# Kernel tuning notes

Measured on AMD Instinct MI355X. Metric: run time of the kernel, lower is better.

The kernel has to match this reference:

```python
import jax, jax.numpy as jnp
import numpy as np
import math

DIM = 1024
N_HEADS = 16
HEAD_DIM = DIM // N_HEADS


def rope(x):
    # x: [B, H, S, D] with D == HEAD_DIM, interleaved even/odd rotation
    S = x.shape[-2]
    D = x.shape[-1]
    pos = jnp.arange(S, dtype=x.dtype)[:, None]              # [S, 1]
    dim = jnp.arange(D // 2, dtype=x.dtype)[None, :]         # [1, D/2]
    theta = pos / jnp.exp(2.0 * dim / D * math.log(10000.0))  # [S, D/2]
    sin = jnp.sin(theta)[None, None]                          # [1,1,S,D/2]
    cos = jnp.cos(theta)[None, None]
    x1 = x[..., ::2]
    x2 = x[..., 1::2]
    out1 = x1 * cos - x2 * sin
    out2 = x1 * sin + x2 * cos
    # interleave back: stack on last axis then flatten pairs
    return jnp.stack([out1, out2], axis=-1).reshape(x.shape)


def setup_inputs() -> dict:
    key = jax.random.key(0)
    ks = jax.random.split(key, 9)
    B, S = 2, 2048
    s = 1.0 / math.sqrt(DIM)
    inp = {
        "x": jax.random.normal(ks[0], (B, S, DIM), dtype=jnp.float32),
        "wq": jax.random.normal(ks[1], (DIM, DIM), dtype=jnp.float32) * s,
        "bq": jnp.zeros((DIM,), dtype=jnp.float32),
        "wk": jax.random.normal(ks[2], (DIM, DIM), dtype=jnp.float32) * s,
        "bk": jnp.zeros((DIM,), dtype=jnp.float32),
        "wv": jax.random.normal(ks[3], (DIM, DIM), dtype=jnp.float32) * s,
        "bv": jnp.zeros((DIM,), dtype=jnp.float32),
        "wo": jax.random.normal(ks[4], (DIM, DIM), dtype=jnp.float32) * s,
        "bo": jnp.zeros((DIM,), dtype=jnp.float32),
    }
    return inp


def reference(x, wq, bq, wk, bk, wv, bv, wo, bo):
    B, S, _ = x.shape
    # torch Linear: y = x @ W^T + b
    def proj(w, b):
        y = jnp.einsum('bsd,ed->bse', x, w) + b
        return y.reshape(B, S, N_HEADS, HEAD_DIM).transpose(0, 2, 1, 3)  # [B,H,S,Dh]
    q = rope(proj(wq, bq))
    k = rope(proj(wk, bk))
    v = proj(wv, bv)
    score = jnp.einsum('bhqd,bhkd->bhqk', q, k) / math.sqrt(HEAD_DIM)
    causal = jnp.tril(jnp.ones((S, S), dtype=bool))
    score = jnp.where(causal[None, None], score, -jnp.inf)
    attn = jax.nn.softmax(score, axis=-1)
    out = jnp.einsum('bhqk,bhkd->bhqd', attn, v)
    out = out.transpose(0, 2, 1, 3).reshape(B, S, DIM)
    return jnp.einsum('bsd,ed->bse', out, wo) + bo
```

## Files before the change

kernel.cpp:

```cpp
#include <hip/hip_runtime.h>
#include <cstdint>
#include <cstddef>
#include <cmath>


typedef __bf16 bf16_t;
typedef __bf16 bf16x8 __attribute__((ext_vector_type(8)));
typedef __bf16 bf16x4 __attribute__((ext_vector_type(4)));
typedef float  f32x4  __attribute__((ext_vector_type(4)));

#define DEVFN __device__ __forceinline__

static constexpr int Bn  = 2;
static constexpr int S   = 2048;
static constexpr int DIM = 1024;
static constexpr int NH  = 16;
static constexpr int HD  = 64;
static constexpr int Mrows = Bn * S;

DEVFN f32x4 mfma16(bf16x8 a, bf16x8 b, f32x4 c) {
  return __builtin_amdgcn_mfma_f32_16x16x32_bf16(a, b, c, 0, 0, 0);
}

DEVFN void gl_lds16(const bf16_t* g, bf16_t* l) {
  __builtin_amdgcn_global_load_lds(
      (const __attribute__((address_space(1))) unsigned*)g,
      (__attribute__((address_space(3))) unsigned*)l, 16, 0, 0);
}

DEVFN float fast_exp2(float x) { return exp2f(x); }

__global__ __launch_bounds__(256) void k_prep(
    const float* __restrict__ x, const float* __restrict__ wq,
    const float* __restrict__ wk, const float* __restrict__ wv,
    const float* __restrict__ wo, bf16_t* __restrict__ xb,
    bf16_t* __restrict__ wqb, bf16_t* __restrict__ wkb,
    bf16_t* __restrict__ wvb, bf16_t* __restrict__ wob,
    float2* __restrict__ tab) {
  const int bid = blockIdx.x;
  if (bid < 8192) {
    const float* src;
    bf16_t* dst;
    size_t base;
    if (bid < 4096) {
      src = x; dst = xb; base = (size_t)bid << 10;
    } else {
      int wsel = (bid - 4096) >> 10;
      src = wsel == 0 ? wq : wsel == 1 ? wk : wsel == 2 ? wv : wo;
      dst = wsel == 0 ? wqb : wsel == 1 ? wkb : wsel == 2 ? wvb : wob;
      base = (size_t)((bid - 4096) & 1023) << 10;
    }
    size_t i = base + (size_t)threadIdx.x * 4;
    float4 v = *(const float4*)(src + i);
    bf16x4 o = { (bf16_t)v.x, (bf16_t)v.y, (bf16_t)v.z, (bf16_t)v.w };
    *(bf16x4*)(dst + i) = o;
  } else {
    int i = (bid - 8192) * 256 + threadIdx.x;
    int s = i >> 5, d = i & 31;
    float th = (float)s * expf((float)d * -0.2878231366f);
    tab[i] = make_float2(cosf(th), sinf(th));
  }
}

__global__ __launch_bounds__(256) void k_rope(bf16_t* __restrict__ X,
                                              const float2* __restrict__ tab,
                                              float scale) {
  int i = blockIdx.x * 256 + threadIdx.x;
  int row = i >> 7;
  int s = row & (S - 1);
  int dd = (i & 7) << 3;
  int p0 = dd >> 1;
  bf16x8 v = *(bf16x8*)(X + (size_t)i * 8);
  bf16x8 o;
#pragma unroll
  for (int j = 0; j < 4; ++j) {
    float x1 = (float)v[2 * j], x2 = (float)v[2 * j + 1];
    float2 cs = tab[s * 32 + p0 + j];
    o[2 * j]     = (bf16_t)((x1 * cs.x - x2 * cs.y) * scale);
    o[2 * j + 1] = (bf16_t)((x1 * cs.y + x2 * cs.x) * scale);
  }
  *(bf16x8*)(X + (size_t)i * 8) = o;
}

__global__ __launch_bounds__(256) void k_trans(const bf16_t* __restrict__ Vin,
                                               bf16_t* __restrict__ VT) {
  __shared__ __align__(16) bf16_t tile[64][72];
  int s0 = blockIdx.x * 64, bh = blockIdx.y;
  int b = bh >> 4, h = bh & 15;
  int t = threadIdx.x;
#pragma unroll
  for (int it = 0; it < 2; ++it) {
    int sl = (t >> 3) + it * 32, d0 = (t & 7) << 3;
    *(bf16x8*)&tile[sl][d0] =
        *(const bf16x8*)(Vin + (size_t)(b * S + s0 + sl) * DIM + h * HD + d0);
  }
  __syncthreads();
  int d = t >> 2, c0 = (t & 3) * 16;
  bf16_t buf[16];
#pragma unroll
  for (int j = 0; j < 16; ++j) buf[j] = tile[c0 + j][d];
  bf16_t* op = VT + ((size_t)bh * HD + d) * S + s0 + c0;
  *(bf16x8*)op = *(bf16x8*)&buf[0];
  *(bf16x8*)(op + 8) = *(bf16x8*)&buf[8];
}

DEVFN void stage64(const bf16_t* __restrict__ A, const bf16_t* __restrict__ Bw,
                   bf16_t* Al, bf16_t* Bl, int m0, int n0, int k0, int t,
                   int w) {
#pragma unroll
  for (int ld = 0; ld < 4; ++ld) {
    int c = t + ld * 256;
    int row = c >> 3;
    int j = ((c & 7) ^ (row & 7)) << 3;
    bf16_t* dstA = Al + (size_t)(w * 64 + ld * 256) * 8;
    bf16_t* dstB = Bl + (size_t)(w * 64 + ld * 256) * 8;
    gl_lds16(A + (size_t)(m0 + row) * DIM + k0 + j, dstA);
    gl_lds16(Bw + (size_t)(n0 + row) * DIM + k0 + j, dstB);
  }
}

__global__ __launch_bounds__(256) void k_gemm_qkv(
    const bf16_t* __restrict__ A, const bf16_t* __restrict__ Wall,
    const float* __restrict__ c0, const float* __restrict__ c1,
    const float* __restrict__ c2, bf16_t* __restrict__ Oq,
    bf16_t* __restrict__ Ok, bf16_t* __restrict__ Ov_) {
  __shared__ __align__(16) bf16_t Al[128 * 64];
  __shared__ __align__(16) bf16_t Bl[128 * 64];
  const int t = threadIdx.x, w = t >> 6, l = t & 63;
  const int lr = l & 15, lc = l >> 4;
  const int lid = blockIdx.x;
  const int xcd = lid & 7, s = lid >> 3;
  const int my = ((xcd >> 1) << 3) + (s & 7);
  const int nx = (xcd & 1) * 12 + (s >> 3);
  const int m0 = my * 128, n0g = nx * 128;
  const int z = n0g >> 10, n0l = n0g & 1023;
  const int wr = w >> 1, wc = w & 1;
  f32x4 acc[4][4] = {};

  for (int k0 = 0; k0 < DIM; k0 += 64) {
    __syncthreads();
    stage64(A, Wall, Al, Bl, m0, n0g, k0, t, w);
    asm volatile("s_waitcnt vmcnt(0)" ::: "memory");
    __syncthreads();
    bf16x8 af[2][4], bfr[2][4];
#pragma unroll
    for (int ks = 0; ks < 2; ++ks) {
#pragma unroll
      for (int mi = 0; mi < 4; ++mi) {
        int row = wr * 64 + mi * 16 + lr;
        int off = ((ks * 4 + lc) << 4) ^ ((row & 7) << 4);
        af[ks][mi] = *(const bf16x8*)((const char*)Al + row * 128 + off);
      }
#pragma unroll
      for (int ni = 0; ni < 4; ++ni) {
        int row = wc * 64 + ni * 16 + lr;
        int off = ((ks * 4 + lc) << 4) ^ ((row & 7) << 4);
        bfr[ks][ni] = *(const bf16x8*)((const char*)Bl + row * 128 + off);
      }
    }
    __builtin_amdgcn_s_setprio(1);
#pragma unroll
    for (int ks = 0; ks < 2; ++ks)
#pragma unroll
      for (int mi = 0; mi < 4; ++mi)
#pragma unroll
        for (int ni = 0; ni < 4; ++ni)
          acc[mi][ni] = mfma16(af[ks][mi], bfr[ks][ni], acc[mi][ni]);
    __builtin_amdgcn_s_setprio(0);
  }

  bf16_t* Ov = z == 0 ? Oq : (z == 1 ? Ok : Ov_);
  const float* bias = z == 0 ? c0 : (z == 1 ? c1 : c2);
#pragma unroll
  for (int ni = 0; ni < 4; ++ni) {
    const int col = n0l + wc * 64 + ni * 16 + lr;
    const float bv = bias[col];
#pragma unroll
    for (int mi = 0; mi < 4; ++mi)
#pragma unroll
      for (int r = 0; r < 4; ++r) {
        int row = m0 + wr * 64 + mi * 16 + lc * 4 + r;
        Ov[(size_t)row * DIM + col] = (bf16_t)(acc[mi][ni][r] + bv);
      }
  }
}

__global__ __launch_bounds__(256) void k_gemm_out(
    const bf16_t* __restrict__ A, const bf16_t* __restrict__ Bw,
    const float* __restrict__ bias, float* __restrict__ Ov) {
  __shared__ __align__(16) bf16_t Al[128 * 64];
  __shared__ __align__(16) bf16_t Bl[128 * 64];
  const int t = threadIdx.x, w = t >> 6, l = t & 63;
  const int lr = l & 15, lc = l >> 4;
  const int lid = blockIdx.x;
  const int xcd = lid & 7, s = lid >> 3;
  const int my = ((xcd >> 1) << 3) + (s & 7);
  const int nx = (xcd & 1) * 4 + (s >> 3);
  const int m0 = my * 128, n0 = nx * 128;
  const int wr = w >> 1, wc = w & 1;
  f32x4 acc[4][4] = {};

  for (int k0 = 0; k0 < DIM; k0 += 64) {
    __syncthreads();
    stage64(A, Bw, Al, Bl, m0, n0, k0, t, w);
    asm volatile("s_waitcnt vmcnt(0)" ::: "memory");
    __syncthreads();
    bf16x8 af[2][4], bfr[2][4];
#pragma unroll
    for (int ks = 0; ks < 2; ++ks) {
#pragma unroll
      for (int mi = 0; mi < 4; ++mi) {
        int row = wr * 64 + mi * 16 + lr;
        int off = ((ks * 4 + lc) << 4) ^ ((row & 7) << 4);
        af[ks][mi] = *(const bf16x8*)((const char*)Al + row * 128 + off);
      }
#pragma unroll
      for (int ni = 0; ni < 4; ++ni) {
        int row = wc * 64 + ni * 16 + lr;
        int off = ((ks * 4 + lc) << 4) ^ ((row & 7) << 4);
        bfr[ks][ni] = *(const bf16x8*)((const char*)Bl + row * 128 + off);
      }
    }
    __builtin_amdgcn_s_setprio(1);
#pragma unroll
    for (int ks = 0; ks < 2; ++ks)
#pragma unroll
      for (int mi = 0; mi < 4; ++mi)
#pragma unroll
        for (int ni = 0; ni < 4; ++ni)
          acc[mi][ni] = mfma16(af[ks][mi], bfr[ks][ni], acc[mi][ni]);
    __builtin_amdgcn_s_setprio(0);
  }

#pragma unroll
  for (int ni = 0; ni < 4; ++ni) {
    int col = n0 + wc * 64 + ni * 16 + lr;
    float bv = bias[col];
#pragma unroll
    for (int mi = 0; mi < 4; ++mi)
#pragma unroll
      for (int r = 0; r < 4; ++r) {
        int row = m0 + wr * 64 + mi * 16 + lc * 4 + r;
        Ov[(size_t)row * DIM + col] = acc[mi][ni][r] + bv;
      }
  }
}

DEVFN void stage_kv(const bf16_t* __restrict__ Kc,
                    const bf16_t* __restrict__ VT, bf16_t* Kb, bf16_t* Vb,
                    int b, int bh, int h, int k0, int tid, int w) {
#pragma unroll
  for (int ld = 0; ld < 2; ++ld) {
    int c = tid + ld * 256;
    int row = c >> 3;
    int j = ((c & 7) ^ (row & 7)) << 3;
    bf16_t* dstK = Kb + (size_t)(w * 64 + ld * 256) * 8;
    bf16_t* dstV = Vb + (size_t)(w * 64 + ld * 256) * 8;
    gl_lds16(Kc + (size_t)(b * S + k0 + row) * DIM + h * HD + j, dstK);
    gl_lds16(VT + ((size_t)bh * HD + row) * S + k0 + j, dstV);
  }
}

__global__ __launch_bounds__(256) void k_attn(const bf16_t* __restrict__ Q,
                                              const bf16_t* __restrict__ Kc,
                                              const bf16_t* __restrict__ VT,
                                              bf16_t* __restrict__ O) {
  __shared__ __align__(16) bf16_t Kl[2][64 * 64];
  __shared__ __align__(16) bf16_t Vl[2][64 * 64];
  __shared__ __align__(16) bf16_t Pl[4][16 * 64];
  const int tid = threadIdx.x, w = tid >> 6, l = tid & 63;
  const int lr = l & 15, lc = l >> 4;
  const int lid = blockIdx.x;
  const int xcd = lid & 7;
  const int rest = lid >> 3;
  const int t_ord = rest >> 2;
  const int hh = rest & 3;
  const int tile = 31 - t_ord;
  const int bh = xcd * 4 + hh;
  const int b = bh >> 4, h = bh & 15;
  char* Pw = (char*)&Pl[w][0];

  const int q0 = tile * 64;
  const int nt = tile + 1;

  bf16x8 qf[2];
  {
    const bf16_t* qp =
        Q + (size_t)(b * S + q0 + w * 16 + lr) * DIM + h * HD + lc * 8;
    qf[0] = *(const bf16x8*)qp;
    qf[1] = *(const bf16x8*)(qp + 32);
  }
  f32x4 o[4] = {};
  float m_run = -INFINITY;
  float rowsum = 0.f;

  stage_kv(Kc, VT, &Kl[0][0], &Vl[0][0], b, bh, h, 0, tid, w);

#pragma unroll 1
  for (int it = 0; it < nt; ++it) {
    const int cur = it & 1;
    const bf16_t* Kb = &Kl[cur][0];
    const bf16_t* Vb = &Vl[cur][0];
    if (it + 1 < nt) {
      stage_kv(Kc, VT, &Kl[cur ^ 1][0], &Vl[cur ^ 1][0], b, bh, h,
               (it + 1) * 64, tid, w);
      asm volatile("s_waitcnt vmcnt(4)" ::: "memory");
    } else {
      asm volatile("s_waitcnt vmcnt(0)" ::: "memory");
    }
    __builtin_amdgcn_s_barrier();
    __builtin_amdgcn_sched_barrier(0);

    f32x4 s[4] = {};
    __builtin_amdgcn_s_setprio(1);
#pragma unroll
    for (int ks = 0; ks < 2; ++ks) {
#pragma unroll
      for (int ni = 0; ni < 4; ++ni) {
        int row = ni * 16 + lr;
        int off = (ks * 64 + lc * 16) ^ ((row & 7) << 4);
        bf16x8 kf = *(const bf16x8*)((const char*)Kb + row * 128 + off);
        s[ni] = mfma16(kf, qf[ks], s[ni]);
      }
    }
    __builtin_amdgcn_s_setprio(0);

    if (it == tile) {
      const int qloc = w * 16 + lr;
#pragma unroll
      for (int ni = 0; ni < 4; ++ni)
#pragma unroll
        for (int r = 0; r < 4; ++r)
          if (ni * 16 + lc * 4 + r > qloc) s[ni][r] = -INFINITY;
    }

    float m01 = fmaxf(fmaxf(s[0][0], s[0][1]), fmaxf(s[0][2], s[0][3]));
    float m23 = fmaxf(fmaxf(s[1][0], s[1][1]), fmaxf(s[1][2], s[1][3]));
    float m45 = fmaxf(fmaxf(s[2][0], s[2][1]), fmaxf(s[2][2], s[2][3]));
    float m67 = fmaxf(fmaxf(s[3][0], s[3][1]), fmaxf(s[3][2], s[3][3]));
    float pm = fmaxf(fmaxf(m01, m23), fmaxf(m45, m67));
    pm = fmaxf(pm, __shfl_xor(pm, 16));
    pm = fmaxf(pm, __shfl_xor(pm, 32));

    if (__ballot(pm > m_run + 8.f)) {
      float mn = fmaxf(m_run, pm);
      float alpha = fast_exp2(m_run - mn);
      m_run = mn;
      rowsum *= alpha;
#pragma unroll
      for (int r = 0; r < 4; ++r) {
        float aq = __shfl(alpha, lc * 4 + r);
#pragma unroll
        for (int ni = 0; ni < 4; ++ni) o[ni][r] *= aq;
      }
    }

    float rs = 0.f;
#pragma unroll
    for (int ni = 0; ni < 4; ++ni) {
      float p0 = fast_exp2(s[ni][0] - m_run);
      float p1 = fast_exp2(s[ni][1] - m_run);
      float p2 = fast_exp2(s[ni][2] - m_run);
      float p3 = fast_exp2(s[ni][3] - m_run);
      rs += (p0 + p1) + (p2 + p3);
      bf16x4 pb = { (bf16_t)p0, (bf16_t)p1, (bf16_t)p2, (bf16_t)p3 };
      *(bf16x4*)(Pw + (lr * 128 + ((ni * 32 + lc * 8) ^ ((lr & 7) << 4)))) =
          pb;
    }
    rs += __shfl_xor(rs, 16);
    rs += __shfl_xor(rs, 32);
    rowsum += rs;

    __builtin_amdgcn_s_setprio(1);
#pragma unroll
    for (int ks = 0; ks < 2; ++ks) {
      int off = ks * 64 + lc * 16;
      bf16x8 pa = *(const bf16x8*)(Pw + lr * 128 + (off ^ ((lr & 7) << 4)));
#pragma unroll
      for (int ni = 0; ni < 4; ++ni) {
        int vrow = ni * 16 + lr;
        bf16x8 vb = *(const bf16x8*)((const char*)Vb + vrow * 128 +
                                     (off ^ ((vrow & 7) << 4)));
        o[ni] = mfma16(pa, vb, o[ni]);
      }
    }
    __builtin_amdgcn_s_setprio(0);

    __builtin_amdgcn_s_barrier();
  }

  float inv[4];
#pragma unroll
  for (int r = 0; r < 4; ++r) inv[r] = 1.0f / __shfl(rowsum, lc * 4 + r);
#pragma unroll
  for (int ni = 0; ni < 4; ++ni)
#pragma unroll
    for (int r = 0; r < 4; ++r) {
      int qr = q0 + w * 16 + lc * 4 + r;
      float v = o[ni][r] * inv[r];
      O[(size_t)(b * S + qr) * DIM + h * HD + ni * 16 + lr] = (bf16_t)v;
    }
}

extern "C" void kernel_launch(void* const* d_in, const int* in_sizes, int n_in,
                              void* d_out, int out_size, void* d_ws,
                              size_t ws_size, hipStream_t stream) {
  const float* x  = (const float*)d_in[0];
  const float* wq = (const float*)d_in[1];
  const float* bq = (const float*)d_in[2];
  const float* wk = (const float*)d_in[3];
  const float* bk = (const float*)d_in[4];
  const float* wv = (const float*)d_in[5];
  const float* bv = (const float*)d_in[6];
  const float* wo = (const float*)d_in[7];
  const float* bo = (const float*)d_in[8];

  const size_t MD = (size_t)Mrows * DIM;
  const size_t WD = (size_t)DIM * DIM;
  bf16_t* W = (bf16_t*)d_ws;
  bf16_t* x_bf  = W;
  bf16_t* wq_bf = x_bf + MD;
  bf16_t* wk_bf = wq_bf + WD;
  bf16_t* wv_bf = wk_bf + WD;
  bf16_t* wo_bf = wv_bf + WD;
  bf16_t* q_lin = wo_bf + WD;
  bf16_t* k_lin = q_lin + MD;
  bf16_t* v_lin = k_lin + MD;
  bf16_t* vT    = v_lin + MD;
  float2* tab   = (float2*)(vT + MD);
  bf16_t* attn_out = x_bf;

  k_prep<<<8448, 256, 0, stream>>>(x, wq, wk, wv, wo, x_bf, wq_bf, wk_bf,
                                   wv_bf, wo_bf, tab);

  k_gemm_qkv<<<768, 256, 0, stream>>>(x_bf, wq_bf, bq, bk, bv, q_lin, k_lin,
                                      v_lin);

  k_rope<<<2048, 256, 0, stream>>>(q_lin, tab, 0.125f * 1.4426950408889634f);
  k_rope<<<2048, 256, 0, stream>>>(k_lin, tab, 1.0f);
  k_trans<<<dim3(S / 64, Bn * NH), 256, 0, stream>>>(v_lin, vT);

  k_attn<<<1024, 256, 0, stream>>>(q_lin, k_lin, vT, attn_out);

  k_gemm_out<<<256, 256, 0, stream>>>(attn_out, wo_bf, bo, (float*)d_out);
}
```

Before: 129.6 us.

## Merge rope launches, halve out-GEMM tile width, single-buffer attention K/V

The two RoPE launches become one kernel that picks Q or K by block index, which saves a launch. The output GEMM moves from 128x128 to 128x64 tiles and doubles the grid to 512 blocks, giving more parallelism across CUs at the cost of less reuse per tile. The attention kernel drops its K/V double buffering and loads each tile synchronously. This halves the shared memory it needs and may raise occupancy, but it removes the overlap of loads with compute.

```diff
diff --git a/kernel.cpp b/kernel.cpp
--- a/kernel.cpp
+++ b/kernel.cpp
@@ -62,14 +62,17 @@
   }
 }
 
-__global__ __launch_bounds__(256) void k_rope(bf16_t* __restrict__ X,
-                                              const float2* __restrict__ tab,
-                                              float scale) {
-  int i = blockIdx.x * 256 + threadIdx.x;
+__global__ __launch_bounds__(256) void k_rope2(bf16_t* __restrict__ q,
+                                               bf16_t* __restrict__ k,
+                                               const float2* __restrict__ tab,
+                                               float sq) {
+  const int bid = blockIdx.x;
+  bf16_t* X = bid < 2048 ? q : k;
+  const float scale = bid < 2048 ? sq : 1.0f;
+  int i = (bid & 2047) * 256 + threadIdx.x;
   int row = i >> 7;
   int s = row & (S - 1);
-  int dd = (i & 7) << 3;
-  int p0 = dd >> 1;
+  int p0 = (i & 7) << 2;
   bf16x8 v = *(bf16x8*)(X + (size_t)i * 8);
   bf16x8 o;
 #pragma unroll
@@ -189,34 +192,48 @@
     const bf16_t* __restrict__ A, const bf16_t* __restrict__ Bw,
     const float* __restrict__ bias, float* __restrict__ Ov) {
   __shared__ __align__(16) bf16_t Al[128 * 64];
-  __shared__ __align__(16) bf16_t Bl[128 * 64];
+  __shared__ __align__(16) bf16_t Bl[64 * 64];
   const int t = threadIdx.x, w = t >> 6, l = t & 63;
   const int lr = l & 15, lc = l >> 4;
   const int lid = blockIdx.x;
   const int xcd = lid & 7, s = lid >> 3;
   const int my = ((xcd >> 1) << 3) + (s & 7);
-  const int nx = (xcd & 1) * 4 + (s >> 3);
-  const int m0 = my * 128, n0 = nx * 128;
-  const int wr = w >> 1, wc = w & 1;
-  f32x4 acc[4][4] = {};
+  const int nx = (xcd & 1) * 8 + (s >> 3);
+  const int m0 = my * 128, n0 = nx * 64;
+  f32x4 acc[2][4] = {};
 
   for (int k0 = 0; k0 < DIM; k0 += 64) {
     __syncthreads();
-    stage64(A, Bw, Al, Bl, m0, n0, k0, t, w);
+#pragma unroll
+    for (int ld = 0; ld < 4; ++ld) {
+      int c = t + ld * 256;
+      int row = c >> 3;
+      int j = ((c & 7) ^ (row & 7)) << 3;
+      gl_lds16(A + (size_t)(m0 + row) * DIM + k0 + j,
+               Al + (size_t)(w * 64 + ld * 256) * 8);
+    }
+#pragma unroll
+    for (int ld = 0; ld < 2; ++ld) {
+      int c = t + ld * 256;
+      int row = c >> 3;
+      int j = ((c & 7) ^ (row & 7)) << 3;
+      gl_lds16(Bw + (size_t)(n0 + row) * DIM + k0 + j,
+               Bl + (size_t)(w * 64 + ld * 256) * 8);
+    }
     asm volatile("s_waitcnt vmcnt(0)" ::: "memory");
     __syncthreads();
-    bf16x8 af[2][4], bfr[2][4];
+    bf16x8 af[2][2], bfr[2][4];
 #pragma unroll
     for (int ks = 0; ks < 2; ++ks) {
 #pragma unroll
-      for (int mi = 0; mi < 4; ++mi) {
-        int row = wr * 64 + mi * 16 + lr;
+      for (int mi = 0; mi < 2; ++mi) {
+        int row = w * 32 + mi * 16 + lr;
         int off = ((ks * 4 + lc) << 4) ^ ((row & 7) << 4);
         af[ks][mi] = *(const bf16x8*)((const char*)Al + row * 128 + off);
       }
 #pragma unroll
       for (int ni = 0; ni < 4; ++ni) {
-        int row = wc * 64 + ni * 16 + lr;
+        int row = ni * 16 + lr;
         int off = ((ks * 4 + lc) << 4) ^ ((row & 7) << 4);
         bfr[ks][ni] = *(const bf16x8*)((const char*)Bl + row * 128 + off);
       }
@@ -225,7 +242,7 @@
 #pragma unroll
     for (int ks = 0; ks < 2; ++ks)
 #pragma unroll
-      for (int mi = 0; mi < 4; ++mi)
+      for (int mi = 0; mi < 2; ++mi)
 #pragma unroll
         for (int ni = 0; ni < 4; ++ni)
           acc[mi][ni] = mfma16(af[ks][mi], bfr[ks][ni], acc[mi][ni]);
@@ -234,13 +251,13 @@
 
 #pragma unroll
   for (int ni = 0; ni < 4; ++ni) {
-    int col = n0 + wc * 64 + ni * 16 + lr;
+    int col = n0 + ni * 16 + lr;
     float bv = bias[col];
 #pragma unroll
-    for (int mi = 0; mi < 4; ++mi)
+    for (int mi = 0; mi < 2; ++mi)
 #pragma unroll
       for (int r = 0; r < 4; ++r) {
-        int row = m0 + wr * 64 + mi * 16 + lc * 4 + r;
+        int row = m0 + w * 32 + mi * 16 + lc * 4 + r;
         Ov[(size_t)row * DIM + col] = acc[mi][ni][r] + bv;
       }
   }
@@ -265,8 +282,8 @@
                                               const bf16_t* __restrict__ Kc,
                                               const bf16_t* __restrict__ VT,
                                               bf16_t* __restrict__ O) {
-  __shared__ __align__(16) bf16_t Kl[2][64 * 64];
-  __shared__ __align__(16) bf16_t Vl[2][64 * 64];
+  __shared__ __align__(16) bf16_t Kl[64 * 64];
+  __shared__ __align__(16) bf16_t Vl[64 * 64];
   __shared__ __align__(16) bf16_t Pl[4][16 * 64];
   const int tid = threadIdx.x, w = tid >> 6, l = tid & 63;
   const int lr = l & 15, lc = l >> 4;
@@ -294,20 +311,10 @@
   float m_run = -INFINITY;
   float rowsum = 0.f;
 
-  stage_kv(Kc, VT, &Kl[0][0], &Vl[0][0], b, bh, h, 0, tid, w);
-
 #pragma unroll 1
   for (int it = 0; it < nt; ++it) {
-    const int cur = it & 1;
-    const bf16_t* Kb = &Kl[cur][0];
-    const bf16_t* Vb = &Vl[cur][0];
-    if (it + 1 < nt) {
-      stage_kv(Kc, VT, &Kl[cur ^ 1][0], &Vl[cur ^ 1][0], b, bh, h,
-               (it + 1) * 64, tid, w);
-      asm volatile("s_waitcnt vmcnt(4)" ::: "memory");
-    } else {
-      asm volatile("s_waitcnt vmcnt(0)" ::: "memory");
-    }
+    stage_kv(Kc, VT, &Kl[0], &Vl[0], b, bh, h, it * 64, tid, w);
+    asm volatile("s_waitcnt vmcnt(0)" ::: "memory");
     __builtin_amdgcn_s_barrier();
     __builtin_amdgcn_sched_barrier(0);
 
@@ -319,7 +326,7 @@
       for (int ni = 0; ni < 4; ++ni) {
         int row = ni * 16 + lr;
         int off = (ks * 64 + lc * 16) ^ ((row & 7) << 4);
-        bf16x8 kf = *(const bf16x8*)((const char*)Kb + row * 128 + off);
+        bf16x8 kf = *(const bf16x8*)((const char*)Kl + row * 128 + off);
         s[ni] = mfma16(kf, qf[ks], s[ni]);
       }
     }
@@ -379,7 +386,7 @@
 #pragma unroll
       for (int ni = 0; ni < 4; ++ni) {
         int vrow = ni * 16 + lr;
-        bf16x8 vb = *(const bf16x8*)((const char*)Vb + vrow * 128 +
+        bf16x8 vb = *(const bf16x8*)((const char*)Vl + vrow * 128 +
                                      (off ^ ((vrow & 7) << 4)));
         o[ni] = mfma16(pa, vb, o[ni]);
       }
@@ -436,11 +443,11 @@
   k_gemm_qkv<<<768, 256, 0, stream>>>(x_bf, wq_bf, bq, bk, bv, q_lin, k_lin,
                                       v_lin);
 
-  k_rope<<<2048, 256, 0, stream>>>(q_lin, tab, 0.125f * 1.4426950408889634f);
-  k_rope<<<2048, 256, 0, stream>>>(k_lin, tab, 1.0f);
+  k_rope2<<<4096, 256, 0, stream>>>(q_lin, k_lin, tab,
+                                    0.125f * 1.4426950408889634f);
   k_trans<<<dim3(S / 64, Bn * NH), 256, 0, stream>>>(v_lin, vT);
 
   k_attn<<<1024, 256, 0, stream>>>(q_lin, k_lin, vT, attn_out);
 
-  k_gemm_out<<<256, 256, 0, stream>>>(attn_out, wo_bf, bo, (float*)d_out);
-}
+  k_gemm_out<<<512, 256, 0, stream>>>(attn_out, wo_bf, bo, (float*)d_out);
+}
```

Result: faster. 124.6 us, median of 2 (-3.9%).
